# Kernel tuning notes

Measured on AMD Instinct MI355X. Metric: run time of the kernel, lower is better.

The kernel has to match this reference:

```python
import jax, jax.numpy as jnp
import numpy as np

B, T, H, W = 64, 128, 64, 64
K = 3          # conv kernel size
NH = 64        # hidden_dim == n_qubits (required for the gating math to broadcast)
IN = 1         # input_dim (scalar conv feature per frame)
NC = 10        # num_classes


def setup_inputs() -> dict:
    key = jax.random.key(0)
    ks = jax.random.split(key, 32)
    i = iter(range(32))

    def lin(kw, kb, fan_in, fan_out):
        s = 1.0 / np.sqrt(fan_in)
        w = jax.random.uniform(kw, (fan_out, fan_in), jnp.float32, -s, s)
        b = jax.random.uniform(kb, (fan_out,), jnp.float32, -s, s)
        return w, b

    inp = {"images": jax.random.normal(ks[next(i)], (B, T, 1, H, W), jnp.float32)}
    inp["threshold"] = jnp.float32(0.5)
    s = 1.0 / np.sqrt(K * K)
    inp["conv_w"] = jax.random.uniform(ks[next(i)], (1, 1, K, K), jnp.float32, -s, s)
    inp["conv_b"] = jax.random.uniform(ks[next(i)], (1,), jnp.float32, -s, s)
    for g in ("f", "i", "u", "o"):
        w, b = lin(ks[next(i)], ks[next(i)], IN + NH, NH)
        inp[f"fc_{g}_w"], inp[f"fc_{g}_b"] = w, b
        lw, lb = lin(ks[next(i)], ks[next(i)], NH, NH)
        ew, eb = lin(ks[next(i)], ks[next(i)], NH, NH)
        inp[f"q_{g}_lw"], inp[f"q_{g}_lb"] = lw, lb
        inp[f"q_{g}_ew"], inp[f"q_{g}_eb"] = ew, eb
    inp["cls_w"], inp["cls_b"] = lin(ks[next(i)], ks[next(i)], NH, NC)
    return inp


def _qlayer(x, lw, lb, ew, eb):
    out = jnp.tanh(x @ lw.T + lb)
    return out * jax.nn.sigmoid(out @ ew.T + eb)


def reference(images, threshold, conv_w, conv_b,
              fc_f_w, fc_f_b, fc_i_w, fc_i_b, fc_u_w, fc_u_b, fc_o_w, fc_o_b,
              q_f_lw, q_f_lb, q_f_ew, q_f_eb,
              q_i_lw, q_i_lb, q_i_ew, q_i_eb,
              q_u_lw, q_u_lb, q_u_ew, q_u_eb,
              q_o_lw, q_o_lb, q_o_ew, q_o_eb,
              cls_w, cls_b):
    b, t, c, h, w = images.shape
    nh = q_f_lw.shape[0]
    # ConvFilter over all frames at once (vectorized across batch*time)
    x = images.reshape(b * t, c, h, w)
    logits = jax.lax.conv_general_dilated(
        x, conv_w, (1, 1), "VALID",
        dimension_numbers=("NCHW", "OIHW", "NCHW")) + conv_b[None, :, None, None]
    feat = jax.nn.sigmoid(logits - threshold).mean(axis=(2, 3))  # [B*T, 1]
    seq = feat.reshape(b, t, 1).transpose(1, 0, 2)               # [T, B, 1]

    def step(carry, xt):
        hx, cx = carry
        comb = jnp.concatenate([xt, hx], axis=1)                 # [B, 1+NH]
        f = jax.nn.sigmoid(_qlayer(comb @ fc_f_w.T + fc_f_b, q_f_lw, q_f_lb, q_f_ew, q_f_eb))
        i = jax.nn.sigmoid(_qlayer(comb @ fc_i_w.T + fc_i_b, q_i_lw, q_i_lb, q_i_ew, q_i_eb))
        g = jnp.tanh(_qlayer(comb @ fc_u_w.T + fc_u_b, q_u_lw, q_u_lb, q_u_ew, q_u_eb))
        o = jax.nn.sigmoid(_qlayer(comb @ fc_o_w.T + fc_o_b, q_o_lw, q_o_lb, q_o_ew, q_o_eb))
        cx = f * cx + i * g
        hx = o * jnp.tanh(cx)
        return (hx, cx), hx

    h0 = jnp.zeros((b, nh), images.dtype)
    c0 = jnp.zeros((b, nh), images.dtype)
    _, outs = jax.lax.scan(step, (h0, c0), seq)                  # [T, B, NH]
    return outs @ cls_w.T + cls_b                                # [T, B, NC]
```

## Files before the change

kernel.cpp:

```cpp
#include <hip/hip_runtime.h>

#define T_ 128
#define B_ 64
#define NH_ 64
#define NC_ 10

__device__ __forceinline__ float sigmoid_f(float x) {
    return 1.0f / (1.0f + __expf(-x));
}
__device__ __forceinline__ float tanh_f(float x) {
    return 1.0f - 2.0f / (1.0f + __expf(2.0f * x));
}

__global__ __launch_bounds__(256) void conv_feat(const float* __restrict__ img,
                                                 const float* __restrict__ cw,
                                                 const float* __restrict__ cb,
                                                 const float* __restrict__ thr,
                                                 float* __restrict__ feat) {
    __shared__ __align__(16) float im[64 * 64];
    const int f = blockIdx.x;
    const int tid = threadIdx.x;
    const float* src = img + (size_t)f * 4096;
#pragma unroll
    for (int i = 0; i < 4; i++) {
        *(float4*)&im[(i * 256 + tid) * 4] = *(const float4*)&src[(i * 256 + tid) * 4];
    }
    const float w0 = cw[0], w1 = cw[1], w2 = cw[2], w3 = cw[3], w4 = cw[4],
                w5 = cw[5], w6 = cw[6], w7 = cw[7], w8 = cw[8];
    const float bias = cb[0] - thr[0];
    __syncthreads();

    float sum = 0.0f;
#pragma unroll
    for (int i = 0; i < 16; i++) {
        int idx = i * 256 + tid;
        if (idx < 62 * 62) {
            int oy = idx / 62;
            int ox = idx - oy * 62;
            const float* p = &im[oy * 64 + ox];
            float acc = bias;
            acc = fmaf(p[0],   w0, acc);
            acc = fmaf(p[1],   w1, acc);
            acc = fmaf(p[2],   w2, acc);
            acc = fmaf(p[64],  w3, acc);
            acc = fmaf(p[65],  w4, acc);
            acc = fmaf(p[66],  w5, acc);
            acc = fmaf(p[128], w6, acc);
            acc = fmaf(p[129], w7, acc);
            acc = fmaf(p[130], w8, acc);
            sum += sigmoid_f(acc);
        }
    }
#pragma unroll
    for (int off = 32; off >= 1; off >>= 1) sum += __shfl_down(sum, off, 64);
    __shared__ float wsum[4];
    const int wv = tid >> 6, ln = tid & 63;
    if (ln == 0) wsum[wv] = sum;
    __syncthreads();
    if (tid == 0) feat[f] = (wsum[0] + wsum[1] + wsum[2] + wsum[3]) * (1.0f / 3844.0f);
}

struct FuseArgs {
    const float* fcw[4];
    const float* fcb[4];
    const float* lw[4];
    const float* lb[4];
};

__global__ __launch_bounds__(256) void fuse_kernel(FuseArgs a, float* __restrict__ Aall,
                                                   float* __restrict__ Vall,
                                                   float* __restrict__ Call) {
    const int g = blockIdx.x;
    const float* fcw = a.fcw[g];
    const float* fcb = a.fcb[g];
    const float* lw  = a.lw[g];
    const float* lb  = a.lb[g];
    __shared__ float fcs[64 * 65];
    __shared__ float fbs[64];
    for (int i = threadIdx.x; i < 64 * 65; i += 256) fcs[i] = fcw[i];
    if (threadIdx.x < 64) fbs[threadIdx.x] = fcb[threadIdx.x];
    __syncthreads();

    const int n = threadIdx.x >> 2;
    const int j0 = (threadIdx.x & 3) * 16;
    float lrow[64];
#pragma unroll
    for (int k = 0; k < 64; k++) lrow[k] = lw[n * 64 + k];

    for (int j = j0; j < j0 + 16; j++) {
        float s = 0.0f;
#pragma unroll
        for (int k = 0; k < 64; k++) s = fmaf(lrow[k], fcs[k * 65 + j + 1], s);
        Aall[(g * 64 + n) * 64 + j] = s;
    }
    if ((threadIdx.x & 3) == 0) {
        float sv = 0.0f, sc = 0.0f;
#pragma unroll
        for (int k = 0; k < 64; k++) {
            sv = fmaf(lrow[k], fcs[k * 65], sv);
            sc = fmaf(lrow[k], fbs[k], sc);
        }
        Vall[g * 64 + n] = sv;
        Call[g * 64 + n] = sc + lb[n];
    }
}

__global__ __launch_bounds__(256, 1) void recur(
    const float* __restrict__ feat, const float* __restrict__ Aall,
    const float* __restrict__ Vall, const float* __restrict__ Call,
    const float* __restrict__ ew_f, const float* __restrict__ eb_f,
    const float* __restrict__ ew_i, const float* __restrict__ eb_i,
    const float* __restrict__ ew_u, const float* __restrict__ eb_u,
    const float* __restrict__ ew_o, const float* __restrict__ eb_o,
    float* __restrict__ outs) {
    const int b = blockIdx.x;
    const int tid = threadIdx.x;
    const int g = tid >> 6, n = tid & 63;
    const float* ew  = (g == 0) ? ew_f : (g == 1) ? ew_i : (g == 2) ? ew_u : ew_o;
    const float* ebp = (g == 0) ? eb_f : (g == 1) ? eb_i : (g == 2) ? eb_u : eb_o;

    float W1[64], W2[64];
#pragma unroll
    for (int k4 = 0; k4 < 16; k4++) {
        float4 av = *(const float4*)&Aall[tid * 64 + k4 * 4];
        W1[k4 * 4 + 0] = av.x; W1[k4 * 4 + 1] = av.y;
        W1[k4 * 4 + 2] = av.z; W1[k4 * 4 + 3] = av.w;
        float4 ev = *(const float4*)&ew[n * 64 + k4 * 4];
        W2[k4 * 4 + 0] = ev.x; W2[k4 * 4 + 1] = ev.y;
        W2[k4 * 4 + 2] = ev.z; W2[k4 * 4 + 3] = ev.w;
    }
    const float vj = Vall[tid], cj = Call[tid], ebj = ebp[n];

    __shared__ __align__(16) float hxs[64];
    __shared__ __align__(16) float qs[256];
    __shared__ __align__(16) float acts[256];
    __shared__ float xts[T_];
    for (int i = tid; i < T_; i += 256) xts[i] = feat[b * T_ + i];
    if (tid < 64) hxs[tid] = 0.0f;
    float cx = 0.0f;
    __syncthreads();

    for (int t = 0; t < T_; t++) {
        float a0 = 0, a1 = 0, a2 = 0, a3 = 0;
#pragma unroll
        for (int k4 = 0; k4 < 16; k4++) {
            float4 h = *(const float4*)&hxs[k4 * 4];
            a0 = fmaf(W1[k4 * 4 + 0], h.x, a0);
            a1 = fmaf(W1[k4 * 4 + 1], h.y, a1);
            a2 = fmaf(W1[k4 * 4 + 2], h.z, a2);
            a3 = fmaf(W1[k4 * 4 + 3], h.w, a3);
        }
        const float q = tanh_f(fmaf(xts[t], vj, cj) + ((a0 + a1) + (a2 + a3)));
        qs[tid] = q;
        __syncthreads();

        float s0 = 0, s1 = 0, s2 = 0, s3 = 0;
#pragma unroll
        for (int k4 = 0; k4 < 16; k4++) {
            float4 qv = *(const float4*)&qs[(g << 6) + k4 * 4];
            s0 = fmaf(W2[k4 * 4 + 0], qv.x, s0);
            s1 = fmaf(W2[k4 * 4 + 1], qv.y, s1);
            s2 = fmaf(W2[k4 * 4 + 2], qv.z, s2);
            s3 = fmaf(W2[k4 * 4 + 3], qv.w, s3);
        }
        const float z = q * sigmoid_f(((s0 + s1) + (s2 + s3)) + ebj);
        const float act = (g == 2) ? tanh_f(z) : sigmoid_f(z);
        acts[tid] = act;
        __syncthreads();

        if (tid < 64) {
            const float ff = acts[tid], ii = acts[64 + tid],
                        uu = acts[128 + tid], oo = acts[192 + tid];
            cx = fmaf(ff, cx, ii * uu);
            const float h = oo * tanh_f(cx);
            hxs[tid] = h;
            outs[((size_t)t * B_ + b) * NH_ + tid] = h;
        }
        __syncthreads();
    }
}

__global__ __launch_bounds__(256) void classify(const float* __restrict__ outs,
                                                const float* __restrict__ cw,
                                                const float* __restrict__ cbias,
                                                float* __restrict__ out) {
    const int tid = threadIdx.x;
    const int r = tid >> 6, ln = tid & 63;
    const int row = blockIdx.x * 4 + r;
    const float h = outs[(size_t)row * 64 + ln];
    float p[10];
#pragma unroll
    for (int c = 0; c < 10; c++) p[c] = h * cw[c * 64 + ln];
#pragma unroll
    for (int off = 32; off >= 1; off >>= 1) {
#pragma unroll
        for (int c = 0; c < 10; c++) p[c] += __shfl_xor(p[c], off, 64);
    }
    if (ln < 10) out[(size_t)row * 10 + ln] = p[ln] + cbias[ln];
}

extern "C" void kernel_launch(void* const* d_in, const int* in_sizes, int n_in,
                              void* d_out, int out_size, void* d_ws, size_t ws_size,
                              hipStream_t stream) {
    const float* images = (const float*)d_in[0];
    const float* thr    = (const float*)d_in[1];
    const float* convw  = (const float*)d_in[2];
    const float* convb  = (const float*)d_in[3];
    const float* fcw[4]; const float* fcb[4]; const float* lw[4]; const float* lb[4];
    const float* ew[4];  const float* eb[4];
    for (int g = 0; g < 4; g++) {
        int base = 4 + g * 6;
        fcw[g] = (const float*)d_in[base + 0];
        fcb[g] = (const float*)d_in[base + 1];
        lw[g]  = (const float*)d_in[base + 2];
        lb[g]  = (const float*)d_in[base + 3];
        ew[g]  = (const float*)d_in[base + 4];
        eb[g]  = (const float*)d_in[base + 5];
    }
    const float* clsw = (const float*)d_in[28];
    const float* clsb = (const float*)d_in[29];

    float* ws   = (float*)d_ws;
    float* feat = ws;
    float* Aall = ws + 8192;
    float* Vall = ws + 24576;
    float* Call = ws + 24832;
    float* outs = ws + 25088;

    conv_feat<<<8192, 256, 0, stream>>>(images, convw, convb, thr, feat);

    FuseArgs fa;
    for (int g = 0; g < 4; g++) {
        fa.fcw[g] = fcw[g]; fa.fcb[g] = fcb[g];
        fa.lw[g] = lw[g];   fa.lb[g] = lb[g];
    }
    fuse_kernel<<<4, 256, 0, stream>>>(fa, Aall, Vall, Call);

    recur<<<B_, 256, 0, stream>>>(feat, Aall, Vall, Call,
                                  ew[0], eb[0], ew[1], eb[1],
                                  ew[2], eb[2], ew[3], eb[3], outs);

    classify<<<2048, 256, 0, stream>>>(outs, clsw, clsb, (float*)d_out);
}
```

Baseline: 181.0 us.

## Merge conv and fuse kernels, fold classifier into recurrence, cut per-step barriers

Launches the conv-feature and weight-fusion work as one grid, removing a kernel launch. The recurrence now gives each wave its own copy of h and q, and every wave computes the cell update redundantly. This replaces two of the three per-step __syncthreads with wave-local lgkmcnt waits, and double-buffered activations leave one barrier per step. The classifier is folded into the recurrence using a history kept in shared memory, removing the outs round-trip and the last launch, at the cost of more LDS use per block.

```diff
diff --git a/kernel.cpp b/kernel.cpp
--- a/kernel.cpp
+++ b/kernel.cpp
@@ -12,53 +12,7 @@
     return 1.0f - 2.0f / (1.0f + __expf(2.0f * x));
 }
 
-__global__ __launch_bounds__(256) void conv_feat(const float* __restrict__ img,
-                                                 const float* __restrict__ cw,
-                                                 const float* __restrict__ cb,
-                                                 const float* __restrict__ thr,
-                                                 float* __restrict__ feat) {
-    __shared__ __align__(16) float im[64 * 64];
-    const int f = blockIdx.x;
-    const int tid = threadIdx.x;
-    const float* src = img + (size_t)f * 4096;
-#pragma unroll
-    for (int i = 0; i < 4; i++) {
-        *(float4*)&im[(i * 256 + tid) * 4] = *(const float4*)&src[(i * 256 + tid) * 4];
-    }
-    const float w0 = cw[0], w1 = cw[1], w2 = cw[2], w3 = cw[3], w4 = cw[4],
-                w5 = cw[5], w6 = cw[6], w7 = cw[7], w8 = cw[8];
-    const float bias = cb[0] - thr[0];
-    __syncthreads();
-
-    float sum = 0.0f;
-#pragma unroll
-    for (int i = 0; i < 16; i++) {
-        int idx = i * 256 + tid;
-        if (idx < 62 * 62) {
-            int oy = idx / 62;
-            int ox = idx - oy * 62;
-            const float* p = &im[oy * 64 + ox];
-            float acc = bias;
-            acc = fmaf(p[0],   w0, acc);
-            acc = fmaf(p[1],   w1, acc);
-            acc = fmaf(p[2],   w2, acc);
-            acc = fmaf(p[64],  w3, acc);
-            acc = fmaf(p[65],  w4, acc);
-            acc = fmaf(p[66],  w5, acc);
-            acc = fmaf(p[128], w6, acc);
-            acc = fmaf(p[129], w7, acc);
-            acc = fmaf(p[130], w8, acc);
-            sum += sigmoid_f(acc);
-        }
-    }
-#pragma unroll
-    for (int off = 32; off >= 1; off >>= 1) sum += __shfl_down(sum, off, 64);
-    __shared__ float wsum[4];
-    const int wv = tid >> 6, ln = tid & 63;
-    if (ln == 0) wsum[wv] = sum;
-    __syncthreads();
-    if (tid == 0) feat[f] = (wsum[0] + wsum[1] + wsum[2] + wsum[3]) * (1.0f / 3844.0f);
-}
+#define LGKM_WAIT() asm volatile("s_waitcnt lgkmcnt(0)" ::: "memory")
 
 struct FuseArgs {
     const float* fcw[4];
@@ -67,41 +21,89 @@
     const float* lb[4];
 };
 
-__global__ __launch_bounds__(256) void fuse_kernel(FuseArgs a, float* __restrict__ Aall,
-                                                   float* __restrict__ Vall,
-                                                   float* __restrict__ Call) {
-    const int g = blockIdx.x;
-    const float* fcw = a.fcw[g];
-    const float* fcb = a.fcb[g];
-    const float* lw  = a.lw[g];
-    const float* lb  = a.lb[g];
-    __shared__ float fcs[64 * 65];
-    __shared__ float fbs[64];
-    for (int i = threadIdx.x; i < 64 * 65; i += 256) fcs[i] = fcw[i];
-    if (threadIdx.x < 64) fbs[threadIdx.x] = fcb[threadIdx.x];
-    __syncthreads();
-
-    const int n = threadIdx.x >> 2;
-    const int j0 = (threadIdx.x & 3) * 16;
-    float lrow[64];
-#pragma unroll
-    for (int k = 0; k < 64; k++) lrow[k] = lw[n * 64 + k];
-
-    for (int j = j0; j < j0 + 16; j++) {
-        float s = 0.0f;
-#pragma unroll
-        for (int k = 0; k < 64; k++) s = fmaf(lrow[k], fcs[k * 65 + j + 1], s);
-        Aall[(g * 64 + n) * 64 + j] = s;
-    }
-    if ((threadIdx.x & 3) == 0) {
-        float sv = 0.0f, sc = 0.0f;
-#pragma unroll
-        for (int k = 0; k < 64; k++) {
-            sv = fmaf(lrow[k], fcs[k * 65], sv);
-            sc = fmaf(lrow[k], fbs[k], sc);
-        }
-        Vall[g * 64 + n] = sv;
-        Call[g * 64 + n] = sc + lb[n];
+__global__ __launch_bounds__(256) void conv_fuse(
+    const float* __restrict__ img, const float* __restrict__ cw,
+    const float* __restrict__ cb, const float* __restrict__ thr,
+    float* __restrict__ feat, FuseArgs fa, float* __restrict__ Aall,
+    float* __restrict__ Vall, float* __restrict__ Call) {
+    __shared__ __align__(16) float smem[64 * 65 + 64];
+    const int tid = threadIdx.x;
+
+    if (blockIdx.x < 8192) {
+        float* im = smem;
+        const int f = blockIdx.x;
+        const float* src = img + (size_t)f * 4096;
+#pragma unroll
+        for (int i = 0; i < 4; i++) {
+            *(float4*)&im[(i * 256 + tid) * 4] = *(const float4*)&src[(i * 256 + tid) * 4];
+        }
+        const float w0 = cw[0], w1 = cw[1], w2 = cw[2], w3 = cw[3], w4 = cw[4],
+                    w5 = cw[5], w6 = cw[6], w7 = cw[7], w8 = cw[8];
+        const float bias = cb[0] - thr[0];
+        __syncthreads();
+
+        float sum = 0.0f;
+#pragma unroll
+        for (int i = 0; i < 16; i++) {
+            int idx = i * 256 + tid;
+            if (idx < 62 * 62) {
+                int oy = idx / 62;
+                int ox = idx - oy * 62;
+                const float* p = &im[oy * 64 + ox];
+                float acc = bias;
+                acc = fmaf(p[0],   w0, acc);
+                acc = fmaf(p[1],   w1, acc);
+                acc = fmaf(p[2],   w2, acc);
+                acc = fmaf(p[64],  w3, acc);
+                acc = fmaf(p[65],  w4, acc);
+                acc = fmaf(p[66],  w5, acc);
+                acc = fmaf(p[128], w6, acc);
+                acc = fmaf(p[129], w7, acc);
+                acc = fmaf(p[130], w8, acc);
+                sum += sigmoid_f(acc);
+            }
+        }
+#pragma unroll
+        for (int off = 32; off >= 1; off >>= 1) sum += __shfl_down(sum, off, 64);
+        float* wsum = smem + 4096;
+        const int wv = tid >> 6, ln = tid & 63;
+        if (ln == 0) wsum[wv] = sum;
+        __syncthreads();
+        if (tid == 0) feat[f] = (wsum[0] + wsum[1] + wsum[2] + wsum[3]) * (1.0f / 3844.0f);
+    } else {
+        const int g = blockIdx.x - 8192;
+        const float* fcw = fa.fcw[g];
+        const float* fcb = fa.fcb[g];
+        const float* lw  = fa.lw[g];
+        const float* lb  = fa.lb[g];
+        float* fcs = smem;
+        float* fbs = smem + 64 * 65;
+        for (int i = tid; i < 64 * 65; i += 256) fcs[i] = fcw[i];
+        if (tid < 64) fbs[tid] = fcb[tid];
+        __syncthreads();
+
+        const int n = tid >> 2;
+        const int j0 = (tid & 3) * 16;
+        float lrow[64];
+#pragma unroll
+        for (int k = 0; k < 64; k++) lrow[k] = lw[n * 64 + k];
+
+        for (int j = j0; j < j0 + 16; j++) {
+            float s = 0.0f;
+#pragma unroll
+            for (int k = 0; k < 64; k++) s = fmaf(lrow[k], fcs[k * 65 + j + 1], s);
+            Aall[(g * 64 + n) * 64 + j] = s;
+        }
+        if ((tid & 3) == 0) {
+            float sv = 0.0f, sc = 0.0f;
+#pragma unroll
+            for (int k = 0; k < 64; k++) {
+                sv = fmaf(lrow[k], fcs[k * 65], sv);
+                sc = fmaf(lrow[k], fbs[k], sc);
+            }
+            Vall[g * 64 + n] = sv;
+            Call[g * 64 + n] = sc + lb[n];
+        }
     }
 }
 
@@ -112,7 +114,8 @@
     const float* __restrict__ ew_i, const float* __restrict__ eb_i,
     const float* __restrict__ ew_u, const float* __restrict__ eb_u,
     const float* __restrict__ ew_o, const float* __restrict__ eb_o,
-    float* __restrict__ outs) {
+    const float* __restrict__ cls_w, const float* __restrict__ cls_b,
+    float* __restrict__ out) {
     const int b = blockIdx.x;
     const int tid = threadIdx.x;
     const int g = tid >> 6, n = tid & 63;
@@ -131,12 +134,20 @@
     }
     const float vj = Vall[tid], cj = Call[tid], ebj = ebp[n];
 
-    __shared__ __align__(16) float hxs[64];
-    __shared__ __align__(16) float qs[256];
-    __shared__ __align__(16) float acts[256];
+    __shared__ __align__(16) float hxs[4][64];
+    __shared__ __align__(16) float qs[4][64];
+    __shared__ __align__(16) float acts[2][256];
     __shared__ float xts[T_];
+    __shared__ float hist[T_ * 65];
+    __shared__ float cwts[NC_ * 65 + NC_];
+
     for (int i = tid; i < T_; i += 256) xts[i] = feat[b * T_ + i];
-    if (tid < 64) hxs[tid] = 0.0f;
+    for (int i = tid; i < NC_ * 64; i += 256) {
+        int c = i >> 6, k = i & 63;
+        cwts[c * 65 + k] = cls_w[i];
+    }
+    if (tid < NC_) cwts[NC_ * 65 + tid] = cls_b[tid];
+    hxs[g][n] = 0.0f;
     float cx = 0.0f;
     __syncthreads();
 
@@ -144,59 +155,51 @@
         float a0 = 0, a1 = 0, a2 = 0, a3 = 0;
 #pragma unroll
         for (int k4 = 0; k4 < 16; k4++) {
-            float4 h = *(const float4*)&hxs[k4 * 4];
+            float4 h = *(const float4*)&hxs[g][k4 * 4];
             a0 = fmaf(W1[k4 * 4 + 0], h.x, a0);
             a1 = fmaf(W1[k4 * 4 + 1], h.y, a1);
             a2 = fmaf(W1[k4 * 4 + 2], h.z, a2);
             a3 = fmaf(W1[k4 * 4 + 3], h.w, a3);
         }
         const float q = tanh_f(fmaf(xts[t], vj, cj) + ((a0 + a1) + (a2 + a3)));
-        qs[tid] = q;
-        __syncthreads();
+        qs[g][n] = q;
+        LGKM_WAIT();
 
         float s0 = 0, s1 = 0, s2 = 0, s3 = 0;
 #pragma unroll
         for (int k4 = 0; k4 < 16; k4++) {
-            float4 qv = *(const float4*)&qs[(g << 6) + k4 * 4];
+            float4 qv = *(const float4*)&qs[g][k4 * 4];
             s0 = fmaf(W2[k4 * 4 + 0], qv.x, s0);
             s1 = fmaf(W2[k4 * 4 + 1], qv.y, s1);
             s2 = fmaf(W2[k4 * 4 + 2], qv.z, s2);
             s3 = fmaf(W2[k4 * 4 + 3], qv.w, s3);
         }
         const float z = q * sigmoid_f(((s0 + s1) + (s2 + s3)) + ebj);
-        const float act = (g == 2) ? tanh_f(z) : sigmoid_f(z);
-        acts[tid] = act;
-        __syncthreads();
-
-        if (tid < 64) {
-            const float ff = acts[tid], ii = acts[64 + tid],
-                        uu = acts[128 + tid], oo = acts[192 + tid];
-            cx = fmaf(ff, cx, ii * uu);
-            const float h = oo * tanh_f(cx);
-            hxs[tid] = h;
-            outs[((size_t)t * B_ + b) * NH_ + tid] = h;
-        }
-        __syncthreads();
-    }
-}
-
-__global__ __launch_bounds__(256) void classify(const float* __restrict__ outs,
-                                                const float* __restrict__ cw,
-                                                const float* __restrict__ cbias,
-                                                float* __restrict__ out) {
-    const int tid = threadIdx.x;
-    const int r = tid >> 6, ln = tid & 63;
-    const int row = blockIdx.x * 4 + r;
-    const float h = outs[(size_t)row * 64 + ln];
-    float p[10];
-#pragma unroll
-    for (int c = 0; c < 10; c++) p[c] = h * cw[c * 64 + ln];
-#pragma unroll
-    for (int off = 32; off >= 1; off >>= 1) {
-#pragma unroll
-        for (int c = 0; c < 10; c++) p[c] += __shfl_xor(p[c], off, 64);
-    }
-    if (ln < 10) out[(size_t)row * 10 + ln] = p[ln] + cbias[ln];
+        acts[t & 1][tid] = (g == 2) ? tanh_f(z) : sigmoid_f(z);
+        __syncthreads();
+
+        const float ff = acts[t & 1][n];
+        const float ii = acts[t & 1][64 + n];
+        const float uu = acts[t & 1][128 + n];
+        const float oo = acts[t & 1][192 + n];
+        cx = fmaf(ff, cx, ii * uu);
+        const float h = oo * tanh_f(cx);
+        hxs[g][n] = h;
+        if (g == 0) hist[t * 65 + n] = h;
+        LGKM_WAIT();
+    }
+    __syncthreads();
+
+#pragma unroll
+    for (int j = 0; j < 5; j++) {
+        const int o = j * 256 + tid;
+        const int r = o / 10;
+        const int c = o - r * 10;
+        float s = cwts[NC_ * 65 + c];
+#pragma unroll 16
+        for (int k = 0; k < 64; k++) s = fmaf(hist[r * 65 + k], cwts[c * 65 + k], s);
+        out[((size_t)r * B_ + b) * NC_ + c] = s;
+    }
 }
 
 extern "C" void kernel_launch(void* const* d_in, const int* in_sizes, int n_in,
@@ -225,20 +228,18 @@
     float* Aall = ws + 8192;
     float* Vall = ws + 24576;
     float* Call = ws + 24832;
-    float* outs = ws + 25088;
-
-    conv_feat<<<8192, 256, 0, stream>>>(images, convw, convb, thr, feat);
 
     FuseArgs fa;
     for (int g = 0; g < 4; g++) {
         fa.fcw[g] = fcw[g]; fa.fcb[g] = fcb[g];
         fa.lw[g] = lw[g];   fa.lb[g] = lb[g];
     }
-    fuse_kernel<<<4, 256, 0, stream>>>(fa, Aall, Vall, Call);
+
+    conv_fuse<<<8196, 256, 0, stream>>>(images, convw, convb, thr, feat, fa,
+                                        Aall, Vall, Call);
 
     recur<<<B_, 256, 0, stream>>>(feat, Aall, Vall, Call,
                                   ew[0], eb[0], ew[1], eb[1],
-                                  ew[2], eb[2], ew[3], eb[3], outs);
-
-    classify<<<2048, 256, 0, stream>>>(outs, clsw, clsb, (float*)d_out);
-}
+                                  ew[2], eb[2], ew[3], eb[3],
+                                  clsw, clsb, (float*)d_out);
+}
```

Result: slower. 200.5 us (+10.8%).
